# Kernel optimization log

Measured on AMD Instinct MI355X. Metric: run time of the kernel, lower is better.

## Reference

```python
import jax, jax.numpy as jnp
import numpy as np

B, C, L = 128, 1, 4096


def setup_inputs() -> dict:
    key = jax.random.key(0)
    x_0 = jax.random.normal(key, (B, C, L), dtype=jnp.float32)
    return {"x_0": x_0}


def reference(x_0):
    # Original: per-sample F.conv1d(x, flip(x), padding=L-1).
    # Cross-correlation with a flipped kernel == full linear convolution:
    #   out[b, t] = sum_c sum_i x[b,c,i] * x[b,c,t-i],  t in [0, 2L-2]
    # Vectorized over batch and channels via vmap; summed over channels
    # (conv1d contracts input channels against the weight's channel dim).
    conv = jax.vmap(jax.vmap(lambda a: jnp.convolve(a, a, mode='full')))(x_0)  # [B, C, 2L-1]
    return conv.sum(axis=1)[:, None, :]  # [B, 1, 2L-1]
```

## Files before the change

kernel.cpp:

```cpp
#include <hip/hip_runtime.h>

#define LL    4096
#define OUTL  8191
#define FPAD  272
#define NPDW  2336
#define CB1   2352
#define RB    4704
#define BTOP  5887
#define NGU   971
#define LDSDW 9472

typedef short v8s __attribute__((ext_vector_type(8)));
typedef float v4f __attribute__((ext_vector_type(4)));

__device__ __forceinline__ unsigned bf16b(float f) {
    unsigned u = __builtin_bit_cast(unsigned, f);
    u += 0x7fff + ((u >> 16) & 1);
    return u >> 16;
}

struct Frag { unsigned a[4], a2[4]; uint4 b3, b2, b1, b0; };

__global__ __launch_bounds__(512, 4)
void selfconv_mfma5(const float* __restrict__ xg, float* __restrict__ outg) {
    __shared__ unsigned lds[LDSDW];
    const int tid = threadIdx.x;
    const int blk = blockIdx.x;
    const int b   = blk & 127;
    const int id  = blk >> 7;
    const int rg  = (id == 0) ? 0 : (id == 1) ? 3 : (id == 2) ? 1 : 2;
    const int T0  = rg << 11;
    const float* __restrict__ xb = xg + b * LL;

    for (int idx = tid; idx < 2 * NPDW; idx += 512) {
        int r = idx >= NPDW ? 1 : 0;
        int p = idx - r * NPDW;
        int e = 2 * p + r - FPAD;
        float f0 = (e >= 0 && e < LL) ? xb[e] : 0.f;
        float f1 = (e + 1 >= 0 && e + 1 < LL) ? xb[e + 1] : 0.f;
        lds[(r ? CB1 : 0) + p] = bf16b(f0) | (bf16b(f1) << 16);
    }
    for (int g = tid; g < NGU; g += 512) {
        unsigned w[4];
#pragma unroll
        for (int d = 0; d < 4; ++d) {
            int xlo = BTOP - 8 * g - 2 * d;
            int xhi = xlo - 1;
            float flo = (xlo >= 0 && xlo < LL) ? xb[xlo] : 0.f;
            float fhi = (xhi >= 0 && xhi < LL) ? xb[xhi] : 0.f;
            w[d] = bf16b(flo) | (bf16b(fhi) << 16);
        }
        int P = g ^ ((g >> 4) & 1);
        *(uint4*)&lds[RB + 4 * P] = uint4{w[0], w[1], w[2], w[3]};
    }
    __syncthreads();

    const int wv = tid >> 6, lane = tid & 63, ln16 = lane & 15, q = lane >> 4;

    int mn = 0x7fffffff, mx = -0x7fffffff;
#pragma unroll
    for (int u = 0; u < 2; ++u)
#pragma unroll
        for (int v = 0; v < 4; ++v) {
            int base = T0 + 256 * u + 512 * v;
            int iLo = base - (LL - 1); if (iLo < 0) iLo = 0;
            int iHi = base + 255;      if (iHi > LL - 1) iHi = LL - 1;
            int a = iLo - 256 * u; if (a < mn) mn = a;
            int c2 = iHi - 256 * u; if (c2 > mx) mx = c2;
        }
    const int base_   = mn - 15;
    const int i0start = base_ - ((base_ - 1) & 7);
    const int nch     = ((mx - i0start) >> 5) + 1;
    const int nw      = (nch - wv + 7) >> 3;
    const int i0w     = i0start + 32 * wv;

    const int s0p = i0w + ln16 + 8 * q + FPAD;
    int aw = (s0p >> 1) + ((s0p & 1) ? CB1 : 0);
    const int g3 = (BTOP - T0 - 1536 - 16 * ln16 + i0w + 8 * q) >> 3;
    int bw = RB + 4 * (g3 ^ ((g3 >> 4) & 1));

    v4f a00{0,0,0,0}, a01{0,0,0,0}, a02{0,0,0,0}, a03{0,0,0,0};
    v4f a10{0,0,0,0}, a11{0,0,0,0}, a12{0,0,0,0}, a13{0,0,0,0};

    auto ld = [&](Frag& F, int a, int w) {
        F.a[0]  = lds[a];       F.a[1]  = lds[a + 1];
        F.a[2]  = lds[a + 2];   F.a[3]  = lds[a + 3];
        F.a2[0] = lds[a + 128]; F.a2[1] = lds[a + 129];
        F.a2[2] = lds[a + 130]; F.a2[3] = lds[a + 131];
        F.b3 = *(const uint4*)&lds[w];
        F.b2 = *(const uint4*)&lds[w + 256];
        F.b1 = *(const uint4*)&lds[w + 512];
        F.b0 = *(const uint4*)&lds[w + 768];
    };
    auto mkA = [](const unsigned (&u)[4]) {
        union { unsigned x[4]; v8s s; } z;
        z.x[0] = u[0]; z.x[1] = u[1]; z.x[2] = u[2]; z.x[3] = u[3]; return z.s;
    };
    auto mkB = [](uint4 v) {
        union { unsigned x[4]; v8s s; } z;
        z.x[0] = v.x; z.x[1] = v.y; z.x[2] = v.z; z.x[3] = v.w; return z.s;
    };
    auto cmp = [&](const Frag& F) {
        v8s A0 = mkA(F.a), A1 = mkA(F.a2);
        v8s B0 = mkB(F.b0), B1 = mkB(F.b1), B2 = mkB(F.b2), B3 = mkB(F.b3);
        a00 = __builtin_amdgcn_mfma_f32_16x16x32_bf16(A0, B0, a00, 0, 0, 0);
        a10 = __builtin_amdgcn_mfma_f32_16x16x32_bf16(A1, B0, a10, 0, 0, 0);
        a01 = __builtin_amdgcn_mfma_f32_16x16x32_bf16(A0, B1, a01, 0, 0, 0);
        a11 = __builtin_amdgcn_mfma_f32_16x16x32_bf16(A1, B1, a11, 0, 0, 0);
        a02 = __builtin_amdgcn_mfma_f32_16x16x32_bf16(A0, B2, a02, 0, 0, 0);
        a12 = __builtin_amdgcn_mfma_f32_16x16x32_bf16(A1, B2, a12, 0, 0, 0);
        a03 = __builtin_amdgcn_mfma_f32_16x16x32_bf16(A0, B3, a03, 0, 0, 0);
        a13 = __builtin_amdgcn_mfma_f32_16x16x32_bf16(A1, B3, a13, 0, 0, 0);
    };

    Frag F0, F1;
    int awE = aw, bwE = bw, awO = aw + 128, bwO = bw + 128;
    ld(F0, awE, bwE); awE += 256; bwE += 256;
    ld(F1, awO, bwO); awO += 256; bwO += 256;
    int c = 0;
    for (; c + 2 < nw; c += 2) {
        cmp(F0); ld(F0, awE, bwE); awE += 256; bwE += 256;
        cmp(F1); ld(F1, awO, bwO); awO += 256; bwO += 256;
    }
    cmp(F0);
    if (c + 1 < nw) cmp(F1);

    float* fs = (float*)lds;
    __syncthreads();
    if (wv >= 4) {
        int sb = (wv - 4) * 2304 + lane * 36;
        *(v4f*)&fs[sb]      = a00; *(v4f*)&fs[sb + 4]  = a10;
        *(v4f*)&fs[sb + 8]  = a01; *(v4f*)&fs[sb + 12] = a11;
        *(v4f*)&fs[sb + 16] = a02; *(v4f*)&fs[sb + 20] = a12;
        *(v4f*)&fs[sb + 24] = a03; *(v4f*)&fs[sb + 28] = a13;
    }
    __syncthreads();
    if (wv < 4) {
        int sb = wv * 2304 + lane * 36;
        a00 += *(const v4f*)&fs[sb];      a10 += *(const v4f*)&fs[sb + 4];
        a01 += *(const v4f*)&fs[sb + 8];  a11 += *(const v4f*)&fs[sb + 12];
        a02 += *(const v4f*)&fs[sb + 16]; a12 += *(const v4f*)&fs[sb + 20];
        a03 += *(const v4f*)&fs[sb + 24]; a13 += *(const v4f*)&fs[sb + 28];
    }
    __syncthreads();
    if (wv >= 1 && wv < 4) {
        int sb = (wv - 1) * 2304 + lane * 36;
        *(v4f*)&fs[sb]      = a00; *(v4f*)&fs[sb + 4]  = a10;
        *(v4f*)&fs[sb + 8]  = a01; *(v4f*)&fs[sb + 12] = a11;
        *(v4f*)&fs[sb + 16] = a02; *(v4f*)&fs[sb + 20] = a12;
        *(v4f*)&fs[sb + 24] = a03; *(v4f*)&fs[sb + 28] = a13;
    }
    __syncthreads();
    if (wv == 0) {
#pragma unroll
        for (int s = 0; s < 3; ++s) {
            int sb = s * 2304 + lane * 36;
            a00 += *(const v4f*)&fs[sb];      a10 += *(const v4f*)&fs[sb + 4];
            a01 += *(const v4f*)&fs[sb + 8];  a11 += *(const v4f*)&fs[sb + 12];
            a02 += *(const v4f*)&fs[sb + 16]; a12 += *(const v4f*)&fs[sb + 20];
            a03 += *(const v4f*)&fs[sb + 24]; a13 += *(const v4f*)&fs[sb + 28];
        }
        float* __restrict__ ob = outg + b * OUTL;
        const v4f* accs[8] = {&a00, &a10, &a01, &a11, &a02, &a12, &a03, &a13};
#pragma unroll
        for (int uv = 0; uv < 8; ++uv) {
            int u = uv & 1, v = uv >> 1;
            int tb = T0 + 256 * u + 512 * v + 4 * q + 16 * ln16;
            v4f a = *accs[uv];
#pragma unroll
            for (int r2 = 0; r2 < 4; ++r2)
                if (tb + r2 < OUTL) ob[tb + r2] = a[r2];
        }
    }
}

extern "C" void kernel_launch(void* const* d_in, const int* in_sizes, int n_in,
                              void* d_out, int out_size, void* d_ws, size_t ws_size,
                              hipStream_t stream) {
    const float* x = (const float*)d_in[0];
    float* out = (float*)d_out;
    selfconv_mfma5<<<dim3(512), dim3(512), 0, stream>>>(x, out);
}
```

Measured before the change: 65.21 us.

## Vectorize LDS staging loads, change B swizzle, and vectorize output stores

The staging of the input into LDS now uses float4 global loads, and each thread packs both parity-shifted bf16 copies at once instead of issuing scalar loads per element. The reversed B buffer is rebuilt with vector loads, explicit zero padding and a new XOR swizzle meant to reduce LDS bank conflicts. The MFMA issue order is reversed, and output writes become 16-byte vector stores when a tile lies fully in range. The new addressing and swizzle must stay consistent with the compute-side indexing. The float4 loads assume the source offsets are aligned.

After: 61.45 us. 5.8% less time.

```diff
diff --git a/kernel.cpp b/kernel.cpp
--- a/kernel.cpp
+++ b/kernel.cpp
@@ -7,8 +7,8 @@
 #define CB1   2352
 #define RB    4704
 #define BTOP  5887
-#define NGU   971
-#define LDSDW 9472
+#define NGUP  992
+#define LDSDW 9824
 
 typedef short v8s __attribute__((ext_vector_type(8)));
 typedef float v4f __attribute__((ext_vector_type(4)));
@@ -18,11 +18,18 @@
     u += 0x7fff + ((u >> 16) & 1);
     return u >> 16;
 }
-
-struct Frag { unsigned a[4], a2[4]; uint4 b3, b2, b1, b0; };
+__device__ __forceinline__ unsigned pk(float lo, float hi) {
+    return bf16b(lo) | (bf16b(hi) << 16);
+}
+__device__ __forceinline__ int swz(int g) { return g ^ (((g >> 3) & 3) << 1); }
+
+struct Frag {
+    unsigned x0, x1, x2, x3, y0, y1, y2, y3;
+    uint4 b3, b2, b1, b0;
+};
 
 __global__ __launch_bounds__(512, 4)
-void selfconv_mfma5(const float* __restrict__ xg, float* __restrict__ outg) {
+void selfconv_mfma6(const float* __restrict__ xg, float* __restrict__ outg) {
     __shared__ unsigned lds[LDSDW];
     const int tid = threadIdx.x;
     const int blk = blockIdx.x;
@@ -32,26 +39,44 @@
     const int T0  = rg << 11;
     const float* __restrict__ xb = xg + b * LL;
 
-    for (int idx = tid; idx < 2 * NPDW; idx += 512) {
-        int r = idx >= NPDW ? 1 : 0;
-        int p = idx - r * NPDW;
-        int e = 2 * p + r - FPAD;
-        float f0 = (e >= 0 && e < LL) ? xb[e] : 0.f;
-        float f1 = (e + 1 >= 0 && e + 1 < LL) ? xb[e + 1] : 0.f;
-        lds[(r ? CB1 : 0) + p] = bf16b(f0) | (bf16b(f1) << 16);
-    }
-    for (int g = tid; g < NGU; g += 512) {
-        unsigned w[4];
-#pragma unroll
-        for (int d = 0; d < 4; ++d) {
-            int xlo = BTOP - 8 * g - 2 * d;
-            int xhi = xlo - 1;
-            float flo = (xlo >= 0 && xlo < LL) ? xb[xlo] : 0.f;
-            float fhi = (xhi >= 0 && xhi < LL) ? xb[xhi] : 0.f;
-            w[d] = bf16b(flo) | (bf16b(fhi) << 16);
-        }
-        int P = g ^ ((g >> 4) & 1);
-        *(uint4*)&lds[RB + 4 * P] = uint4{w[0], w[1], w[2], w[3]};
+#pragma unroll
+    for (int rr = 0; rr < 2; ++rr) {
+        int w = tid + rr * 512;
+        if (w < 584) {
+            int E = 8 * w - FPAD;
+            float e0,e1,e2,e3,e4,e5,e6,e7,e8;
+            if (E >= 0 && E + 8 < LL) {
+                float4 fa = *(const float4*)(xb + E);
+                float4 fb = *(const float4*)(xb + E + 4);
+                e0=fa.x; e1=fa.y; e2=fa.z; e3=fa.w;
+                e4=fb.x; e5=fb.y; e6=fb.z; e7=fb.w; e8=xb[E+8];
+            } else {
+                float t[9];
+#pragma unroll
+                for (int k = 0; k < 9; ++k) {
+                    int e = E + k;
+                    t[k] = (e >= 0 && e < LL) ? xb[e] : 0.f;
+                }
+                e0=t[0]; e1=t[1]; e2=t[2]; e3=t[3]; e4=t[4];
+                e5=t[5]; e6=t[6]; e7=t[7]; e8=t[8];
+            }
+            uint4 d0{pk(e0,e1), pk(e2,e3), pk(e4,e5), pk(e6,e7)};
+            uint4 d1{pk(e1,e2), pk(e3,e4), pk(e5,e6), pk(e7,e8)};
+            *(uint4*)&lds[4 * w]       = d0;
+            *(uint4*)&lds[CB1 + 4 * w] = d1;
+        }
+    }
+    {
+        int g = 224 + tid;
+        int x0 = BTOP - 7 - 8 * g;
+        float4 fa = *(const float4*)(xb + x0);
+        float4 fb = *(const float4*)(xb + x0 + 4);
+        uint4 o{pk(fb.w, fb.z), pk(fb.y, fb.x), pk(fa.w, fa.z), pk(fa.y, fa.x)};
+        *(uint4*)&lds[RB + 4 * swz(g)] = o;
+    }
+    if (tid < 480) {
+        int u = (tid < 224) ? tid : tid + 512;
+        *(uint4*)&lds[RB + 4 * u] = uint4{0, 0, 0, 0};
     }
     __syncthreads();
 
@@ -75,42 +100,43 @@
     const int i0w     = i0start + 32 * wv;
 
     const int s0p = i0w + ln16 + 8 * q + FPAD;
-    int aw = (s0p >> 1) + ((s0p & 1) ? CB1 : 0);
-    const int g3 = (BTOP - T0 - 1536 - 16 * ln16 + i0w + 8 * q) >> 3;
-    int bw = RB + 4 * (g3 ^ ((g3 >> 4) & 1));
+    const int aw  = (s0p >> 1) + ((s0p & 1) ? CB1 : 0);
+    const int g3 = (4352 - T0 + i0w - 16 * ln16 + 8 * q) >> 3;
+    const int bw = RB + 4 * swz(g3);
 
     v4f a00{0,0,0,0}, a01{0,0,0,0}, a02{0,0,0,0}, a03{0,0,0,0};
     v4f a10{0,0,0,0}, a11{0,0,0,0}, a12{0,0,0,0}, a13{0,0,0,0};
 
     auto ld = [&](Frag& F, int a, int w) {
-        F.a[0]  = lds[a];       F.a[1]  = lds[a + 1];
-        F.a[2]  = lds[a + 2];   F.a[3]  = lds[a + 3];
-        F.a2[0] = lds[a + 128]; F.a2[1] = lds[a + 129];
-        F.a2[2] = lds[a + 130]; F.a2[3] = lds[a + 131];
+        F.x0 = lds[a];       F.x1 = lds[a + 1];
+        F.x2 = lds[a + 2];   F.x3 = lds[a + 3];
+        F.y0 = lds[a + 128]; F.y1 = lds[a + 129];
+        F.y2 = lds[a + 130]; F.y3 = lds[a + 131];
         F.b3 = *(const uint4*)&lds[w];
         F.b2 = *(const uint4*)&lds[w + 256];
         F.b1 = *(const uint4*)&lds[w + 512];
         F.b0 = *(const uint4*)&lds[w + 768];
     };
-    auto mkA = [](const unsigned (&u)[4]) {
+    auto mkA = [](unsigned u0, unsigned u1, unsigned u2, unsigned u3) {
         union { unsigned x[4]; v8s s; } z;
-        z.x[0] = u[0]; z.x[1] = u[1]; z.x[2] = u[2]; z.x[3] = u[3]; return z.s;
+        z.x[0] = u0; z.x[1] = u1; z.x[2] = u2; z.x[3] = u3; return z.s;
     };
     auto mkB = [](uint4 v) {
         union { unsigned x[4]; v8s s; } z;
         z.x[0] = v.x; z.x[1] = v.y; z.x[2] = v.z; z.x[3] = v.w; return z.s;
     };
     auto cmp = [&](const Frag& F) {
-        v8s A0 = mkA(F.a), A1 = mkA(F.a2);
-        v8s B0 = mkB(F.b0), B1 = mkB(F.b1), B2 = mkB(F.b2), B3 = mkB(F.b3);
+        v8s A0 = mkA(F.x0, F.x1, F.x2, F.x3);
+        v8s A1 = mkA(F.y0, F.y1, F.y2, F.y3);
+        v8s B3 = mkB(F.b3), B2 = mkB(F.b2), B1 = mkB(F.b1), B0 = mkB(F.b0);
+        a03 = __builtin_amdgcn_mfma_f32_16x16x32_bf16(A0, B3, a03, 0, 0, 0);
+        a13 = __builtin_amdgcn_mfma_f32_16x16x32_bf16(A1, B3, a13, 0, 0, 0);
+        a02 = __builtin_amdgcn_mfma_f32_16x16x32_bf16(A0, B2, a02, 0, 0, 0);
+        a12 = __builtin_amdgcn_mfma_f32_16x16x32_bf16(A1, B2, a12, 0, 0, 0);
+        a01 = __builtin_amdgcn_mfma_f32_16x16x32_bf16(A0, B1, a01, 0, 0, 0);
+        a11 = __builtin_amdgcn_mfma_f32_16x16x32_bf16(A1, B1, a11, 0, 0, 0);
         a00 = __builtin_amdgcn_mfma_f32_16x16x32_bf16(A0, B0, a00, 0, 0, 0);
         a10 = __builtin_amdgcn_mfma_f32_16x16x32_bf16(A1, B0, a10, 0, 0, 0);
-        a01 = __builtin_amdgcn_mfma_f32_16x16x32_bf16(A0, B1, a01, 0, 0, 0);
-        a11 = __builtin_amdgcn_mfma_f32_16x16x32_bf16(A1, B1, a11, 0, 0, 0);
-        a02 = __builtin_amdgcn_mfma_f32_16x16x32_bf16(A0, B2, a02, 0, 0, 0);
-        a12 = __builtin_amdgcn_mfma_f32_16x16x32_bf16(A1, B2, a12, 0, 0, 0);
-        a03 = __builtin_amdgcn_mfma_f32_16x16x32_bf16(A0, B3, a03, 0, 0, 0);
-        a13 = __builtin_amdgcn_mfma_f32_16x16x32_bf16(A1, B3, a13, 0, 0, 0);
     };
 
     Frag F0, F1;
@@ -165,11 +191,16 @@
 #pragma unroll
         for (int uv = 0; uv < 8; ++uv) {
             int u = uv & 1, v = uv >> 1;
-            int tb = T0 + 256 * u + 512 * v + 4 * q + 16 * ln16;
+            int tilebase = T0 + 256 * u + 512 * v;
+            int tb = tilebase + 4 * q + 16 * ln16;
             v4f a = *accs[uv];
-#pragma unroll
-            for (int r2 = 0; r2 < 4; ++r2)
-                if (tb + r2 < OUTL) ob[tb + r2] = a[r2];
+            if (tilebase + 255 < OUTL) {
+                *(v4f*)&ob[tb] = a;
+            } else {
+#pragma unroll
+                for (int r2 = 0; r2 < 4; ++r2)
+                    if (tb + r2 < OUTL) ob[tb + r2] = a[r2];
+            }
         }
     }
 }
@@ -179,5 +210,5 @@
                               hipStream_t stream) {
     const float* x = (const float*)d_in[0];
     float* out = (float*)d_out;
-    selfconv_mfma5<<<dim3(512), dim3(512), 0, stream>>>(x, out);
-}
+    selfconv_mfma6<<<dim3(512), dim3(512), 0, stream>>>(x, out);
+}
```
